# Kernel optimization log

Measured on AMD Instinct MI355X. Metric: run time of the kernel, lower is better.

Reference implementation:

```python
import jax, jax.numpy as jnp
import numpy as np

ALPHA = 5.0
EPS = 1e-12  # avoids inf grad of sqrt at the self-distance (exact 0)


def setup_inputs() -> dict:
    key = jax.random.key(0)
    xyz = jax.random.normal(key, (4, 8192, 3), dtype=jnp.float32)
    return {"xyz": xyz, "nbr_size": 2}


def reference(xyz, nbr_size):
    # Brute-force KNN of xyz against itself (self is included with dist 0,
    # matching pointops.knn(query, ref) when query == ref).
    sq = jnp.sum(xyz * xyz, axis=-1)                      # (B, N)
    # squared pairwise distances: ||a||^2 + ||b||^2 - 2 a.b  -> (B, N, N)
    d2 = sq[:, :, None] + sq[:, None, :] - 2.0 * jnp.einsum(
        'bnd,bmd->bnm', xyz, xyz)
    neg_top, _idx = jax.lax.top_k(-d2, nbr_size)          # (B, N, k) smallest d2
    dist = jnp.sqrt(jnp.maximum(-neg_top, EPS))           # Euclidean distance
    dsum = dist.sum(-1)                                   # (B, N)
    avg_dist = dsum.mean(-1, keepdims=True)               # (B, 1)
    # loss = sum of per-point distance sums exceeding alpha * mean
    loss = jnp.where(dsum > avg_dist * ALPHA, dsum, 0.0).sum()
    return loss
```

## Files before the change

kernel.cpp:

```cpp
#include <hip/hip_runtime.h>

#define BB 4
#define NN 8192
#define BN (BB * NN)
#define ALPHA 5.0f
#define EPSF 1e-12f
#define BLOCK 256
#define QPT 4
#define QB (BLOCK * QPT)
#define BIGF 1e30f

__device__ __forceinline__ float fmin3f(float a, float b, float c) {
  float d;
  asm("v_min3_f32 %0, %1, %2, %3" : "=v"(d) : "v"(a), "v"(b), "v"(c));
  return d;
}

__global__ __launch_bounds__(BLOCK) void prep_kernel(
    const float* __restrict__ xyz, float4* __restrict__ refs4) {
  int g = blockIdx.x * BLOCK + threadIdx.x;
  float x = xyz[3 * g + 0], y = xyz[3 * g + 1], z = xyz[3 * g + 2];
  float hpp = 0.5f * fmaf(x, x, fmaf(y, y, z * z));
  refs4[g] = make_float4(x, y, z, hpp);
}

template <int NSEG>
__global__ __launch_bounds__(BLOCK, 8) void knn_kernel(
    const float4* __restrict__ refs4, float* __restrict__ pairs) {
  constexpr int SEG = NN / NSEG;
  constexpr int CHUNKS = NN / QB;
  constexpr int U = 8;
  int bid = blockIdx.x;
  int s = bid % NSEG;
  int rem = bid / NSEG;
  int qchunk = rem % CHUNKS;
  int b = rem / CHUNKS;

  const float4* __restrict__ qb4 = refs4 + (size_t)b * NN;

  float nqx[QPT], nqy[QPT], nqz[QPT], hq[QPT], m1[QPT], m2[QPT];
#pragma unroll
  for (int i = 0; i < QPT; i++) {
    int q = qchunk * QB + threadIdx.x + i * BLOCK;
    float4 qp = qb4[q];
    nqx[i] = -qp.x;
    nqy[i] = -qp.y;
    nqz[i] = -qp.z;
    hq[i] = qp.w;
    m1[i] = BIGF;
    m2[i] = BIGF;
  }

  const float4* __restrict__ rp = qb4 + s * SEG;
  const bool self_block = ((s * SEG) / QB) == qchunk;

  float4 cur[U];
#pragma unroll
  for (int u = 0; u < U; u++) cur[u] = rp[u];

  if (!self_block) {
    for (int j0 = 0; j0 < SEG; j0 += U) {
      int jn = (j0 + U < SEG) ? (j0 + U) : 0;
      float4 nxt[U];
#pragma unroll
      for (int u = 0; u < U; u++) nxt[u] = rp[jn + u];

#pragma unroll
      for (int u = 0; u < U; u += 2) {
        float4 p0 = cur[u], p1 = cur[u + 1];
        float pw0 = p0.w, pw1 = p1.w;
#pragma unroll
        for (int i = 0; i < QPT; i++) {
          float t0 = fmaf(nqx[i], p0.x, pw0);
          t0 = fmaf(nqy[i], p0.y, t0);
          t0 = fmaf(nqz[i], p0.z, t0);
          float t1 = fmaf(nqx[i], p1.x, pw1);
          t1 = fmaf(nqy[i], p1.y, t1);
          t1 = fmaf(nqz[i], p1.z, t1);
          m1[i] = fmin3f(m1[i], t0, t1);
        }
      }
#pragma unroll
      for (int u = 0; u < U; u++) cur[u] = nxt[u];
    }
  } else {
    for (int j0 = 0; j0 < SEG; j0 += U) {
      int jn = (j0 + U < SEG) ? (j0 + U) : 0;
      float4 nxt[U];
#pragma unroll
      for (int u = 0; u < U; u++) nxt[u] = rp[jn + u];

#pragma unroll
      for (int u = 0; u < U; u += 2) {
        float4 p0 = cur[u], p1 = cur[u + 1];
        float pw0 = p0.w, pw1 = p1.w;
#pragma unroll
        for (int i = 0; i < QPT; i++) {
          float t0 = fmaf(nqx[i], p0.x, pw0);
          t0 = fmaf(nqy[i], p0.y, t0);
          t0 = fmaf(nqz[i], p0.z, t0);
          float t1 = fmaf(nqx[i], p1.x, pw1);
          t1 = fmaf(nqy[i], p1.y, t1);
          t1 = fmaf(nqz[i], p1.z, t1);
          float med = __builtin_amdgcn_fmed3f(m1[i], t0, t1);
          m2[i] = fminf(m2[i], med);
          m1[i] = fmin3f(m1[i], t0, t1);
        }
      }
#pragma unroll
      for (int u = 0; u < U; u++) cur[u] = nxt[u];
    }
  }

#pragma unroll
  for (int i = 0; i < QPT; i++) {
    int q = qchunk * QB + threadIdx.x + i * BLOCK;
    float best = m1[i];
    if (self_block && (q / SEG) == s) best = m2[i];
    pairs[(size_t)s * BN + b * NN + q] = best + hq[i];
  }
}

#define MBLK 128
#define NPART (BN / MBLK)
template <int NSEG>
__global__ __launch_bounds__(MBLK) void merge_kernel(
    const float* __restrict__ pairs, float* __restrict__ dsum,
    float* __restrict__ partial) {
  int g = blockIdx.x * MBLK + threadIdx.x;
  float m = BIGF;
#pragma unroll 8
  for (int s = 0; s < NSEG; s += 2) {
    float a = pairs[(size_t)s * BN + g];
    float c = pairs[(size_t)(s + 1) * BN + g];
    m = fmin3f(m, a, c);
  }
  float ds = sqrtf(fmaxf(m + m, EPSF)) + sqrtf(EPSF);
  dsum[g] = ds;

  float v = ds;
#pragma unroll
  for (int off = 32; off > 0; off >>= 1) v += __shfl_down(v, off, 64);
  __shared__ float warp_sums[MBLK / 64];
  if ((threadIdx.x & 63) == 0) warp_sums[threadIdx.x >> 6] = v;
  __syncthreads();
  if (threadIdx.x == 0) {
    float t = 0.0f;
#pragma unroll
    for (int w = 0; w < MBLK / 64; w++) t += warp_sums[w];
    partial[blockIdx.x] = t;
  }
}

#define LBLK 1024
__global__ __launch_bounds__(LBLK) void loss_kernel(
    const float* __restrict__ dsum, const float* __restrict__ partial,
    float* __restrict__ out) {
  __shared__ float s_avg[BB];
  if (threadIdx.x < NPART) {
    float v = partial[threadIdx.x];
#pragma unroll
    for (int off = 32; off > 0; off >>= 1) v += __shfl_down(v, off, 64);
    if ((threadIdx.x & 63) == 0) s_avg[threadIdx.x >> 6] = v * (ALPHA / NN);
  }
  __syncthreads();

  const float4* d4 = (const float4*)dsum;
  float acc = 0.0f;
#pragma unroll
  for (int it = 0; it < BN / (LBLK * 4); it++) {
    int idx = it * LBLK + threadIdx.x;
    float4 v = d4[idx];
    float thr = s_avg[idx >> 11];
    acc += (v.x > thr) ? v.x : 0.0f;
    acc += (v.y > thr) ? v.y : 0.0f;
    acc += (v.z > thr) ? v.z : 0.0f;
    acc += (v.w > thr) ? v.w : 0.0f;
  }
#pragma unroll
  for (int off = 32; off > 0; off >>= 1) acc += __shfl_down(acc, off, 64);
  __shared__ float warp_sums[LBLK / 64];
  if ((threadIdx.x & 63) == 0) warp_sums[threadIdx.x >> 6] = acc;
  __syncthreads();
  if (threadIdx.x == 0) {
    float t = 0.0f;
#pragma unroll
    for (int w = 0; w < LBLK / 64; w++) t += warp_sums[w];
    out[0] = t;
  }
}

template <int NSEG>
static void run(const float* xyz, float* out, void* d_ws, hipStream_t stream) {
  float* pairs = (float*)d_ws;
  float4* refs4 = (float4*)(pairs + (size_t)NSEG * BN);
  float* dsum = (float*)(refs4 + BN);
  float* partial = dsum + BN;
  prep_kernel<<<BN / BLOCK, BLOCK, 0, stream>>>(xyz, refs4);
  int grid1 = BB * (NN / QB) * NSEG;
  knn_kernel<NSEG><<<grid1, BLOCK, 0, stream>>>(refs4, pairs);
  merge_kernel<NSEG><<<BN / MBLK, MBLK, 0, stream>>>(pairs, dsum, partial);
  loss_kernel<<<1, LBLK, 0, stream>>>(dsum, partial, out);
}

extern "C" void kernel_launch(void* const* d_in, const int* in_sizes, int n_in,
                              void* d_out, int out_size, void* d_ws,
                              size_t ws_size, hipStream_t stream) {
  const float* xyz = (const float*)d_in[0];
  float* out = (float*)d_out;

  auto need = [](int nseg) {
    return (size_t)nseg * BN * sizeof(float) + BN * sizeof(float4) +
           BN * sizeof(float) + NPART * sizeof(float);
  };
  if (ws_size >= need(64)) {
    run<64>(xyz, out, d_ws, stream);
  } else if (ws_size >= need(32)) {
    run<32>(xyz, out, d_ws, stream);
  } else {
    run<16>(xyz, out, d_ws, stream);
  }
}
```

Baseline: 97.43 us.

## Use packed FP32 FMA with paired reference layout and fuse loss into merge

Prep now also writes the reference points in a paired layout (x0,x1,y0,y1,...), so the KNN inner loop can evaluate two references per query with v_pk_fma_f32, taking reference operands from scalar registers because they are uniform across the wavefront. This is meant to halve the number of FMA issues in the compute-bound distance loop. The separate single-block loss kernel is removed. Instead, the last merge block, found through an atomic counter, performs the final threshold reduction, which saves one launch. This adds workspace, inline asm with SGPR operand constraints, and a last-block synchronization pattern.

```diff
diff --git a/kernel.cpp b/kernel.cpp
--- a/kernel.cpp
+++ b/kernel.cpp
@@ -10,6 +10,10 @@
 #define QB (BLOCK * QPT)
 #define BIGF 1e30f
 
+struct __align__(16) RefPk {
+  float2 x, y, z, w;
+};
+
 __device__ __forceinline__ float fmin3f(float a, float b, float c) {
   float d;
   asm("v_min3_f32 %0, %1, %2, %3" : "=v"(d) : "v"(a), "v"(b), "v"(c));
@@ -17,19 +21,68 @@
 }
 
 __global__ __launch_bounds__(BLOCK) void prep_kernel(
-    const float* __restrict__ xyz, float4* __restrict__ refs4) {
+    const float* __restrict__ xyz, float4* __restrict__ refs4,
+    float* __restrict__ refs_pk, unsigned* __restrict__ counter) {
   int g = blockIdx.x * BLOCK + threadIdx.x;
+  if (g == 0) *counter = 0u;
   float x = xyz[3 * g + 0], y = xyz[3 * g + 1], z = xyz[3 * g + 2];
   float hpp = 0.5f * fmaf(x, x, fmaf(y, y, z * z));
   refs4[g] = make_float4(x, y, z, hpp);
-}
+  float* bp = refs_pk + (size_t)(g >> 1) * 8 + (g & 1);
+  bp[0] = x;
+  bp[2] = y;
+  bp[4] = z;
+  bp[6] = hpp;
+}
+
+#define U2 4
+
+#define LOADPK(dst, J) \
+  _Pragma("unroll") for (int k = 0; k < U2; k++) dst[k] = rp[(J) + k];
+
+#define COMP1(buf)                                                            \
+  _Pragma("unroll") for (int k = 0; k < U2; k++) {                            \
+    float2 rx = buf[k].x, ry = buf[k].y, rz = buf[k].z;                       \
+    float2 w01 = buf[k].w; \
+    _Pragma("unroll") for (int i = 0; i < QPT; i++) {                         \
+      float2 t;                                                               \
+      asm("v_pk_fma_f32 %0, %1, %2, %3"                                       \
+          : "=v"(t)                                                           \
+          : "v"(nqx2[i]), "s"(rx), "v"(w01));                                 \
+      asm("v_pk_fma_f32 %0, %1, %2, %0" : "+v"(t) : "v"(nqy2[i]), "s"(ry));  \
+      asm("v_pk_fma_f32 %0, %1, %2, %0" : "+v"(t) : "v"(nqz2[i]), "s"(rz));  \
+      asm("v_min3_f32 %0, %0, %1, %2"                                         \
+          : "+v"(m1[i])                                                       \
+          : "v"(t.x), "v"(t.y));                                              \
+    }                                                                         \
+  }
+
+#define COMP2(buf)                                                            \
+  _Pragma("unroll") for (int k = 0; k < U2; k++) {                            \
+    float2 rx = buf[k].x, ry = buf[k].y, rz = buf[k].z;                       \
+    float2 w01 = buf[k].w;                                                    \
+    _Pragma("unroll") for (int i = 0; i < QPT; i++) {                         \
+      float2 t;                                                               \
+      asm("v_pk_fma_f32 %0, %1, %2, %3"                                       \
+          : "=v"(t)                                                           \
+          : "v"(nqx2[i]), "s"(rx), "v"(w01));                                 \
+      asm("v_pk_fma_f32 %0, %1, %2, %0" : "+v"(t) : "v"(nqy2[i]), "s"(ry));  \
+      asm("v_pk_fma_f32 %0, %1, %2, %0" : "+v"(t) : "v"(nqz2[i]), "s"(rz));  \
+      float med = __builtin_amdgcn_fmed3f(m1[i], t.x, t.y);       \
+      m2[i] = fminf(m2[i], med);                                              \
+      asm("v_min3_f32 %0, %0, %1, %2"                                         \
+          : "+v"(m1[i])                                                       \
+          : "v"(t.x), "v"(t.y));                                              \
+    }                                                                         \
+  }
 
 template <int NSEG>
 __global__ __launch_bounds__(BLOCK, 8) void knn_kernel(
-    const float4* __restrict__ refs4, float* __restrict__ pairs) {
+    const float4* __restrict__ refs4, const RefPk* __restrict__ refs_pk,
+    float* __restrict__ pairs) {
   constexpr int SEG = NN / NSEG;
+  constexpr int HALF = SEG / 2;
   constexpr int CHUNKS = NN / QB;
-  constexpr int U = 8;
   int bid = blockIdx.x;
   int s = bid % NSEG;
   int rem = bid / NSEG;
@@ -38,77 +91,40 @@
 
   const float4* __restrict__ qb4 = refs4 + (size_t)b * NN;
 
-  float nqx[QPT], nqy[QPT], nqz[QPT], hq[QPT], m1[QPT], m2[QPT];
+  float2 nqx2[QPT], nqy2[QPT], nqz2[QPT];
+  float hq[QPT], m1[QPT], m2[QPT];
 #pragma unroll
   for (int i = 0; i < QPT; i++) {
     int q = qchunk * QB + threadIdx.x + i * BLOCK;
     float4 qp = qb4[q];
-    nqx[i] = -qp.x;
-    nqy[i] = -qp.y;
-    nqz[i] = -qp.z;
+    nqx2[i] = make_float2(-qp.x, -qp.x);
+    nqy2[i] = make_float2(-qp.y, -qp.y);
+    nqz2[i] = make_float2(-qp.z, -qp.z);
     hq[i] = qp.w;
     m1[i] = BIGF;
     m2[i] = BIGF;
   }
 
-  const float4* __restrict__ rp = qb4 + s * SEG;
+  const RefPk* __restrict__ rp = refs_pk + ((size_t)b * NN + s * SEG) / 2;
   const bool self_block = ((s * SEG) / QB) == qchunk;
 
-  float4 cur[U];
-#pragma unroll
-  for (int u = 0; u < U; u++) cur[u] = rp[u];
-
+  RefPk bufA[U2], bufB[U2];
+  LOADPK(bufA, 0);
   if (!self_block) {
-    for (int j0 = 0; j0 < SEG; j0 += U) {
-      int jn = (j0 + U < SEG) ? (j0 + U) : 0;
-      float4 nxt[U];
-#pragma unroll
-      for (int u = 0; u < U; u++) nxt[u] = rp[jn + u];
-
-#pragma unroll
-      for (int u = 0; u < U; u += 2) {
-        float4 p0 = cur[u], p1 = cur[u + 1];
-        float pw0 = p0.w, pw1 = p1.w;
-#pragma unroll
-        for (int i = 0; i < QPT; i++) {
-          float t0 = fmaf(nqx[i], p0.x, pw0);
-          t0 = fmaf(nqy[i], p0.y, t0);
-          t0 = fmaf(nqz[i], p0.z, t0);
-          float t1 = fmaf(nqx[i], p1.x, pw1);
-          t1 = fmaf(nqy[i], p1.y, t1);
-          t1 = fmaf(nqz[i], p1.z, t1);
-          m1[i] = fmin3f(m1[i], t0, t1);
-        }
-      }
-#pragma unroll
-      for (int u = 0; u < U; u++) cur[u] = nxt[u];
+    for (int j = 0; j < HALF; j += 2 * U2) {
+      LOADPK(bufB, j + U2);
+      COMP1(bufA);
+      int jn = (j + 2 * U2 < HALF) ? (j + 2 * U2) : 0;
+      LOADPK(bufA, jn);
+      COMP1(bufB);
     }
   } else {
-    for (int j0 = 0; j0 < SEG; j0 += U) {
-      int jn = (j0 + U < SEG) ? (j0 + U) : 0;
-      float4 nxt[U];
-#pragma unroll
-      for (int u = 0; u < U; u++) nxt[u] = rp[jn + u];
-
-#pragma unroll
-      for (int u = 0; u < U; u += 2) {
-        float4 p0 = cur[u], p1 = cur[u + 1];
-        float pw0 = p0.w, pw1 = p1.w;
-#pragma unroll
-        for (int i = 0; i < QPT; i++) {
-          float t0 = fmaf(nqx[i], p0.x, pw0);
-          t0 = fmaf(nqy[i], p0.y, t0);
-          t0 = fmaf(nqz[i], p0.z, t0);
-          float t1 = fmaf(nqx[i], p1.x, pw1);
-          t1 = fmaf(nqy[i], p1.y, t1);
-          t1 = fmaf(nqz[i], p1.z, t1);
-          float med = __builtin_amdgcn_fmed3f(m1[i], t0, t1);
-          m2[i] = fminf(m2[i], med);
-          m1[i] = fmin3f(m1[i], t0, t1);
-        }
-      }
-#pragma unroll
-      for (int u = 0; u < U; u++) cur[u] = nxt[u];
+    for (int j = 0; j < HALF; j += 2 * U2) {
+      LOADPK(bufB, j + U2);
+      COMP2(bufA);
+      int jn = (j + 2 * U2 < HALF) ? (j + 2 * U2) : 0;
+      LOADPK(bufA, jn);
+      COMP2(bufB);
     }
   }
 
@@ -121,12 +137,13 @@
   }
 }
 
-#define MBLK 128
-#define NPART (BN / MBLK)
+#define MBLK 256
+#define MGRID (BN / MBLK)
 template <int NSEG>
 __global__ __launch_bounds__(MBLK) void merge_kernel(
     const float* __restrict__ pairs, float* __restrict__ dsum,
-    float* __restrict__ partial) {
+    float* __restrict__ partial, unsigned* __restrict__ counter,
+    float* __restrict__ out) {
   int g = blockIdx.x * MBLK + threadIdx.x;
   float m = BIGF;
 #pragma unroll 8
@@ -150,42 +167,47 @@
     for (int w = 0; w < MBLK / 64; w++) t += warp_sums[w];
     partial[blockIdx.x] = t;
   }
-}
-
-#define LBLK 1024
-__global__ __launch_bounds__(LBLK) void loss_kernel(
-    const float* __restrict__ dsum, const float* __restrict__ partial,
-    float* __restrict__ out) {
+
+  __threadfence();
+  __shared__ int s_last;
+  if (threadIdx.x == 0) {
+    unsigned old = atomicAdd(counter, 1u);
+    s_last = (old == (unsigned)(gridDim.x - 1));
+  }
+  __syncthreads();
+  if (!s_last) return;
+  __threadfence();
+
   __shared__ float s_avg[BB];
-  if (threadIdx.x < NPART) {
-    float v = partial[threadIdx.x];
-#pragma unroll
-    for (int off = 32; off > 0; off >>= 1) v += __shfl_down(v, off, 64);
-    if ((threadIdx.x & 63) == 0) s_avg[threadIdx.x >> 6] = v * (ALPHA / NN);
-  }
+  float pv = 0.0f;
+  if (threadIdx.x < MGRID) pv = partial[threadIdx.x];
+#pragma unroll
+  for (int off = 16; off > 0; off >>= 1) pv += __shfl_down(pv, off, 32);
+  if (threadIdx.x < MGRID && (threadIdx.x & 31) == 0)
+    s_avg[threadIdx.x >> 5] = pv * (ALPHA / NN);
   __syncthreads();
 
   const float4* d4 = (const float4*)dsum;
   float acc = 0.0f;
 #pragma unroll
-  for (int it = 0; it < BN / (LBLK * 4); it++) {
-    int idx = it * LBLK + threadIdx.x;
-    float4 v = d4[idx];
+  for (int it = 0; it < BN / (MBLK * 4); it++) {
+    int idx = it * MBLK + threadIdx.x;
+    float4 vv = d4[idx];
     float thr = s_avg[idx >> 11];
-    acc += (v.x > thr) ? v.x : 0.0f;
-    acc += (v.y > thr) ? v.y : 0.0f;
-    acc += (v.z > thr) ? v.z : 0.0f;
-    acc += (v.w > thr) ? v.w : 0.0f;
+    acc += (vv.x > thr) ? vv.x : 0.0f;
+    acc += (vv.y > thr) ? vv.y : 0.0f;
+    acc += (vv.z > thr) ? vv.z : 0.0f;
+    acc += (vv.w > thr) ? vv.w : 0.0f;
   }
 #pragma unroll
   for (int off = 32; off > 0; off >>= 1) acc += __shfl_down(acc, off, 64);
-  __shared__ float warp_sums[LBLK / 64];
-  if ((threadIdx.x & 63) == 0) warp_sums[threadIdx.x >> 6] = acc;
+  __shared__ float w2[MBLK / 64];
+  if ((threadIdx.x & 63) == 0) w2[threadIdx.x >> 6] = acc;
   __syncthreads();
   if (threadIdx.x == 0) {
     float t = 0.0f;
 #pragma unroll
-    for (int w = 0; w < LBLK / 64; w++) t += warp_sums[w];
+    for (int w = 0; w < MBLK / 64; w++) t += w2[w];
     out[0] = t;
   }
 }
@@ -194,13 +216,16 @@
 static void run(const float* xyz, float* out, void* d_ws, hipStream_t stream) {
   float* pairs = (float*)d_ws;
   float4* refs4 = (float4*)(pairs + (size_t)NSEG * BN);
-  float* dsum = (float*)(refs4 + BN);
+  RefPk* refs_pk = (RefPk*)(refs4 + BN);
+  float* dsum = (float*)(refs_pk + BN / 2);
   float* partial = dsum + BN;
-  prep_kernel<<<BN / BLOCK, BLOCK, 0, stream>>>(xyz, refs4);
+  unsigned* counter = (unsigned*)(partial + MGRID);
+  prep_kernel<<<BN / BLOCK, BLOCK, 0, stream>>>(xyz, refs4, (float*)refs_pk,
+                                                counter);
   int grid1 = BB * (NN / QB) * NSEG;
-  knn_kernel<NSEG><<<grid1, BLOCK, 0, stream>>>(refs4, pairs);
-  merge_kernel<NSEG><<<BN / MBLK, MBLK, 0, stream>>>(pairs, dsum, partial);
-  loss_kernel<<<1, LBLK, 0, stream>>>(dsum, partial, out);
+  knn_kernel<NSEG><<<grid1, BLOCK, 0, stream>>>(refs4, refs_pk, pairs);
+  merge_kernel<NSEG><<<BN / MBLK, MBLK, 0, stream>>>(pairs, dsum, partial,
+                                                     counter, out);
 }
 
 extern "C" void kernel_launch(void* const* d_in, const int* in_sizes, int n_in,
@@ -211,7 +236,8 @@
 
   auto need = [](int nseg) {
     return (size_t)nseg * BN * sizeof(float) + BN * sizeof(float4) +
-           BN * sizeof(float) + NPART * sizeof(float);
+           (BN / 2) * sizeof(RefPk) + BN * sizeof(float) +
+           MGRID * sizeof(float) + sizeof(unsigned);
   };
   if (ws_size >= need(64)) {
     run<64>(xyz, out, d_ws, stream);
```

After: 104.3 us. +7.1%, slower.
